# Performance work log

Hardware: AMD Instinct MI355X
Metric: run time of the kernel (lower is better)

## Reference

```python
import jax, jax.numpy as jnp
import numpy as np

D_MODEL = 1024
HEADS = 16


def setup_inputs() -> dict:
    key = jax.random.key(0)
    ks = jax.random.split(key, 5)
    S = 4096
    x = jax.random.normal(ks[0], (S, D_MODEL), dtype=jnp.float32)
    scale = 1.0 / np.sqrt(D_MODEL)
    Wq = jax.random.normal(ks[1], (D_MODEL, D_MODEL), dtype=jnp.float32) * scale
    Wk = jax.random.normal(ks[2], (D_MODEL, D_MODEL), dtype=jnp.float32) * scale
    Wv = jax.random.normal(ks[3], (D_MODEL, D_MODEL), dtype=jnp.float32) * scale
    Wo = jax.random.normal(ks[4], (D_MODEL, D_MODEL), dtype=jnp.float32) * scale
    return {"x": x, "Wq": Wq, "Wk": Wk, "Wv": Wv, "Wo": Wo}


def reference(x, Wq, Wk, Wv, Wo):
    # x: [S, D]; weights follow torch Linear convention y = x @ W.T
    S, D = x.shape
    H = HEADS
    d_k = D // H
    q = (x @ Wq.T).reshape(S, H, d_k)  # [S,H,dk]
    k = (x @ Wk.T).reshape(S, H, d_k)
    v = (x @ Wv.T).reshape(S, H, d_k)
    # logits: [H, S, S] = q k^T / sqrt(d_k)
    logits = jnp.einsum('shd,thd->hst', q, k) / jnp.sqrt(jnp.asarray(d_k, x.dtype))
    probs = jax.nn.softmax(logits, axis=-1)
    out = jnp.einsum('hst,thd->shd', probs, v).reshape(S, D)
    return out @ Wo.T
```

## Files before the change

kernel.cpp:

```cpp
#include <hip/hip_runtime.h>
#include <hip/hip_bf16.h>


typedef __bf16 bf16_t;
typedef __bf16 bf16x8 __attribute__((ext_vector_type(8)));
typedef __bf16 bf16x4 __attribute__((ext_vector_type(4)));
typedef float f32x4 __attribute__((ext_vector_type(4)));

#define D_MODEL 1024
#define SEQ 4096
#define HEADS 16
#define DK 64
#define QSCALE 0.1803368801111204f

__global__ void cast_kernel(const float* __restrict__ in, bf16_t* __restrict__ out, int n) {
    int i = (blockIdx.x * blockDim.x + threadIdx.x) * 4;
    if (i < n) {
        float4 v = *(const float4*)(in + i);
        bf16x4 o;
        o[0] = (bf16_t)v.x; o[1] = (bf16_t)v.y; o[2] = (bf16_t)v.z; o[3] = (bf16_t)v.w;
        *(bf16x4*)(out + i) = o;
    }
}

__global__ void cast4_kernel(const float* __restrict__ a, const float* __restrict__ b,
                             const float* __restrict__ c, const float* __restrict__ d,
                             bf16_t* __restrict__ out) {
    int gi = blockIdx.x * blockDim.x + threadIdx.x;
    int which = gi >> 18;
    int i = (gi & 0x3FFFF) * 4;
    const float* src = which == 0 ? a : which == 1 ? b : which == 2 ? c : d;
    float4 v = *(const float4*)(src + i);
    bf16x4 o;
    o[0] = (bf16_t)v.x; o[1] = (bf16_t)v.y; o[2] = (bf16_t)v.z; o[3] = (bf16_t)v.w;
    *(bf16x4*)(out + (size_t)which * D_MODEL * D_MODEL + i) = o;
}

__device__ __forceinline__ void g2l16(const bf16_t* g, bf16_t* l) {
    __builtin_amdgcn_global_load_lds(
        (const __attribute__((address_space(1))) void*)g,
        (__attribute__((address_space(3))) void*)l, 16, 0, 0);
}

template <int ROUTE>
__global__ __launch_bounds__(256, 4) void gemm_lds(const bf16_t* __restrict__ A,
                                                   const bf16_t* __restrict__ B,
                                                   void* __restrict__ out0,
                                                   void* __restrict__ out1,
                                                   void* __restrict__ out2,
                                                   int M, int N, int K) {
    __shared__ __align__(16) bf16_t As[128 * 64];
    __shared__ __align__(16) bf16_t Bs[64 * 64];

    const int tid = threadIdx.x;
    const int lane = tid & 63;
    const int wave = tid >> 6;
    const int l15 = lane & 15;
    const int lg  = lane >> 4;
    const int m0 = blockIdx.y * 128;
    const int n0 = blockIdx.x * 64;
    const int wm = (wave >> 1) * 64;
    const int wn = (wave & 1) * 32;

    const bf16_t* aSrc[4]; bf16_t* aDst[4];
#pragma unroll
    for (int it = 0; it < 4; it++) {
        int c = it * 256 + tid;
        int row = c >> 3, cc = (c & 7) ^ (row & 7);
        aSrc[it] = A + (size_t)(m0 + row) * K + cc * 8;
        aDst[it] = As + c * 8;
    }
    const bf16_t* bSrc[2]; bf16_t* bDst[2];
#pragma unroll
    for (int it = 0; it < 2; it++) {
        int c = it * 256 + tid;
        int row = c >> 3, cc = (c & 7) ^ (row & 7);
        bSrc[it] = B + (size_t)(n0 + row) * K + cc * 8;
        bDst[it] = Bs + c * 8;
    }

    int aoff[2][4], boff[2][2];
#pragma unroll
    for (int kk = 0; kk < 2; kk++) {
#pragma unroll
        for (int i = 0; i < 4; i++) {
            int row = wm + i * 16 + l15;
            aoff[kk][i] = row * 64 + (((kk << 2) | lg) ^ (row & 7)) * 8;
        }
#pragma unroll
        for (int j = 0; j < 2; j++) {
            int row = wn + j * 16 + l15;
            boff[kk][j] = row * 64 + (((kk << 2) | lg) ^ (row & 7)) * 8;
        }
    }

    f32x4 acc[4][2];
#pragma unroll
    for (int i = 0; i < 4; i++)
#pragma unroll
        for (int j = 0; j < 2; j++) acc[i][j] = f32x4{0.f, 0.f, 0.f, 0.f};

    for (int k0 = 0; k0 < K; k0 += 64) {
#pragma unroll
        for (int it = 0; it < 4; it++) g2l16(aSrc[it] + k0, aDst[it]);
#pragma unroll
        for (int it = 0; it < 2; it++) g2l16(bSrc[it] + k0, bDst[it]);
        __syncthreads();

#pragma unroll
        for (int kk = 0; kk < 2; kk++) {
            bf16x8 af[4], bfm[2];
#pragma unroll
            for (int i = 0; i < 4; i++) af[i] = *(const bf16x8*)(As + aoff[kk][i]);
#pragma unroll
            for (int j = 0; j < 2; j++) bfm[j] = *(const bf16x8*)(Bs + boff[kk][j]);
#pragma unroll
            for (int i = 0; i < 4; i++)
#pragma unroll
                for (int j = 0; j < 2; j++)
                    acc[i][j] = __builtin_amdgcn_mfma_f32_16x16x32_bf16(af[i], bfm[j], acc[i][j], 0, 0, 0);
        }
        __syncthreads();
    }

    const int ng = n0 + wn;
    if (ROUTE == 0) {
        float* C = (float*)out0;
#pragma unroll
        for (int i = 0; i < 4; i++)
#pragma unroll
            for (int r = 0; r < 4; r++) {
                int m = m0 + wm + i * 16 + lg * 4 + r;
                float* crow = C + (size_t)m * N + ng;
#pragma unroll
                for (int j = 0; j < 2; j++) crow[j * 16 + l15] = acc[i][j][r];
            }
    } else {
        if (ng < 2048) {
            const bool isQ = (ng < 1024);
            const float sc = isQ ? QSCALE : 1.0f;
            bf16_t* dst = isQ ? (bf16_t*)out0 : (bf16_t*)out1;
            int nn = ng & 1023;
#pragma unroll
            for (int i = 0; i < 4; i++)
#pragma unroll
                for (int r = 0; r < 4; r++) {
                    int m = m0 + wm + i * 16 + lg * 4 + r;
                    bf16_t* crow = dst + (size_t)m * D_MODEL + nn;
#pragma unroll
                    for (int j = 0; j < 2; j++) crow[j * 16 + l15] = (bf16_t)(acc[i][j][r] * sc);
                }
        } else {
            bf16_t* Vt = (bf16_t*)out2;
#pragma unroll
            for (int i = 0; i < 4; i++)
#pragma unroll
                for (int j = 0; j < 2; j++) {
                    int vcol = ng - 2048 + j * 16 + l15;
                    int m = m0 + wm + i * 16 + lg * 4;
                    bf16x4 v4;
#pragma unroll
                    for (int r = 0; r < 4; r++) v4[r] = (bf16_t)acc[i][j][r];
                    *(bf16x4*)(Vt + (size_t)vcol * SEQ + m) = v4;
                }
        }
    }
}

__global__ __launch_bounds__(256) void attn_kernel(const bf16_t* __restrict__ Q,
                                                   const bf16_t* __restrict__ Km,
                                                   const bf16_t* __restrict__ Vt,
                                                   bf16_t* __restrict__ O) {
    const int tid = threadIdx.x;
    const int lane = tid & 63;
    const int wave = tid >> 6;
    const int l15 = lane & 15;
    const int lg  = lane >> 4;
    const int bid = blockIdx.x;
    const int h    = (bid & 7) * 2 + ((bid >> 3) & 1);
    const int qblk = bid >> 4;
    const int q0 = qblk * 128;
    const int hoff = h * DK;

    __shared__ union {
        struct { __align__(16) bf16_t K[64 * 64]; __align__(16) bf16_t V[64 * 64]; } kv;
        __align__(16) bf16_t Ot[128][72];
    } sm;

    bf16x8 qf[2][2];
#pragma unroll
    for (int t = 0; t < 2; t++)
#pragma unroll
        for (int c = 0; c < 2; c++)
            qf[t][c] = *(const bf16x8*)(Q + (size_t)(q0 + wave * 32 + t * 16 + l15) * D_MODEL
                                        + hoff + c * 32 + lg * 8);

    f32x4 oacc[2][4], lfrag[2];
#pragma unroll
    for (int t = 0; t < 2; t++) {
        lfrag[t] = f32x4{0.f, 0.f, 0.f, 0.f};
#pragma unroll
        for (int dt = 0; dt < 4; dt++) oacc[t][dt] = f32x4{0.f, 0.f, 0.f, 0.f};
    }

    bf16x8 ones8;
#pragma unroll
    for (int j = 0; j < 8; j++) ones8[j] = (bf16_t)1.0f;

    const bf16_t* kSrc[2]; const bf16_t* vSrc[2];
#pragma unroll
    for (int it = 0; it < 2; it++) {
        int c = it * 256 + tid;
        int row = c >> 3, dc = (c & 7) ^ (row & 7);
        kSrc[it] = Km + (size_t)row * D_MODEL + hoff + dc * 8;
        vSrc[it] = Vt + (size_t)(hoff + row) * SEQ + dc * 8;
    }

    int kOff[4][2], vOff[2][2][4];
#pragma unroll
    for (int kt = 0; kt < 4; kt++)
#pragma unroll
        for (int c = 0; c < 2; c++) {
            int row = kt * 16 + l15;
            kOff[kt][c] = row * 64 + (((c * 4 + lg) ^ (row & 7)) * 8);
        }
#pragma unroll
    for (int kp = 0; kp < 2; kp++)
#pragma unroll
        for (int hf = 0; hf < 2; hf++)
#pragma unroll
            for (int dt = 0; dt < 4; dt++) {
                int row = dt * 16 + l15;
                vOff[kp][hf][dt] = row * 64 + (((kp * 4 + hf * 2 + (lg >> 1)) ^ (row & 7)) * 8)
                                   + (lg & 1) * 4;
            }

    for (int s = 0; s < SEQ / 64; s++) {
#pragma unroll
        for (int it = 0; it < 2; it++) {
            g2l16(kSrc[it] + (size_t)s * 64 * D_MODEL, sm.kv.K + (it * 256 + tid) * 8);
            g2l16(vSrc[it] + s * 64,                   sm.kv.V + (it * 256 + tid) * 8);
        }
        __syncthreads();

#pragma unroll
        for (int kp = 0; kp < 2; kp++) {
            f32x4 st[2][2];
#pragma unroll
            for (int sub = 0; sub < 2; sub++) {
                const int kt = kp * 2 + sub;
                const bf16x8 kf0 = *(const bf16x8*)(sm.kv.K + kOff[kt][0]);
                const bf16x8 kf1 = *(const bf16x8*)(sm.kv.K + kOff[kt][1]);
#pragma unroll
                for (int t = 0; t < 2; t++) {
                    f32x4 a = f32x4{0.f, 0.f, 0.f, 0.f};
                    a = __builtin_amdgcn_mfma_f32_16x16x32_bf16(kf0, qf[t][0], a, 0, 0, 0);
                    a = __builtin_amdgcn_mfma_f32_16x16x32_bf16(kf1, qf[t][1], a, 0, 0, 0);
                    st[t][sub] = a;
                }
            }

            bf16x8 pbig[2];
#pragma unroll
            for (int t = 0; t < 2; t++) {
#pragma unroll
                for (int r = 0; r < 4; r++) {
                    pbig[t][r]     = (bf16_t)__builtin_amdgcn_exp2f(st[t][0][r]);
                    pbig[t][r + 4] = (bf16_t)__builtin_amdgcn_exp2f(st[t][1][r]);
                }
            }

            lfrag[0] = __builtin_amdgcn_mfma_f32_16x16x32_bf16(ones8, pbig[0], lfrag[0], 0, 0, 0);
            lfrag[1] = __builtin_amdgcn_mfma_f32_16x16x32_bf16(ones8, pbig[1], lfrag[1], 0, 0, 0);

#pragma unroll
            for (int dt = 0; dt < 4; dt++) {
                const bf16x4 v0 = *(const bf16x4*)(sm.kv.V + vOff[kp][0][dt]);
                const bf16x4 v1 = *(const bf16x4*)(sm.kv.V + vOff[kp][1][dt]);
                bf16x8 vf;
#pragma unroll
                for (int j = 0; j < 4; j++) { vf[j] = v0[j]; vf[j + 4] = v1[j]; }
                oacc[0][dt] = __builtin_amdgcn_mfma_f32_16x16x32_bf16(vf, pbig[0], oacc[0][dt], 0, 0, 0);
                oacc[1][dt] = __builtin_amdgcn_mfma_f32_16x16x32_bf16(vf, pbig[1], oacc[1][dt], 0, 0, 0);
            }
        }
        __syncthreads();
    }

#pragma unroll
    for (int t = 0; t < 2; t++) {
        float inv = 1.f / lfrag[t][0];
        const int qrow = wave * 32 + t * 16 + l15;
#pragma unroll
        for (int dt = 0; dt < 4; dt++)
#pragma unroll
            for (int r = 0; r < 4; r++)
                sm.Ot[qrow][dt * 16 + lg * 4 + r] = (bf16_t)(oacc[t][dt][r] * inv);
    }
    __syncthreads();

    {
        const int row = tid >> 1;
        const int half = tid & 1;
        bf16_t* orow = O + (size_t)(q0 + row) * D_MODEL + hoff + half * 32;
#pragma unroll
        for (int m = 0; m < 4; m++)
            *(bf16x8*)(orow + m * 8) = *(const bf16x8*)(&sm.Ot[row][half * 32 + m * 8]);
    }
}

extern "C" void kernel_launch(void* const* d_in, const int* in_sizes, int n_in,
                              void* d_out, int out_size, void* d_ws, size_t ws_size,
                              hipStream_t stream) {
    const float* x  = (const float*)d_in[0];
    const float* Wq = (const float*)d_in[1];
    const float* Wk = (const float*)d_in[2];
    const float* Wv = (const float*)d_in[3];
    const float* Wo = (const float*)d_in[4];
    float* out = (float*)d_out;

    char* ws = (char*)d_ws;
    bf16_t* xb  = (bf16_t*)(ws);
    bf16_t* wqb = (bf16_t*)(ws + (8u  << 20));
    bf16_t* wob = (bf16_t*)(ws + (14u << 20));
    bf16_t* Qb  = (bf16_t*)(ws + (16u << 20));
    bf16_t* Kb  = (bf16_t*)(ws + (24u << 20));
    bf16_t* Vtb = (bf16_t*)(ws + (32u << 20));
    bf16_t* Ab  = (bf16_t*)(ws + (40u << 20));

    const int nX = SEQ * D_MODEL;
    cast_kernel<<<nX / 4 / 256, 256, 0, stream>>>(x, xb, nX);
    cast4_kernel<<<4 * 1024, 256, 0, stream>>>(Wq, Wk, Wv, Wo, wqb);

    gemm_lds<1><<<dim3(3 * D_MODEL / 64, SEQ / 128), 256, 0, stream>>>(
        xb, wqb, Qb, Kb, Vtb, SEQ, 3 * D_MODEL, D_MODEL);

    attn_kernel<<<512, 256, 0, stream>>>(Qb, Kb, Vtb, Ab);

    gemm_lds<0><<<dim3(D_MODEL / 64, SEQ / 128), 256, 0, stream>>>(
        Ab, wob, out, nullptr, nullptr, SEQ, D_MODEL, D_MODEL);
}
```

Baseline: 226.5 us.

## Split attention over key halves and combine partial outputs in separate kernel

Each attention block now handles only half of the key sequence, doubling the grid to 1024 blocks. Unnormalized partial outputs (bf16) and row sums (fp32) go to workspace, and a new combine kernel adds them, normalizes, and writes the attention output. This is meant to raise occupancy and shorten each block's serial key loop. In exchange it adds an extra launch, extra global traffic for the partials, and bf16 rounding of unnormalized partials.

After: 235.0 us. 1.04x slower.

```diff
diff --git a/kernel.cpp b/kernel.cpp
--- a/kernel.cpp
+++ b/kernel.cpp
@@ -170,7 +170,8 @@
 __global__ __launch_bounds__(256) void attn_kernel(const bf16_t* __restrict__ Q,
                                                    const bf16_t* __restrict__ Km,
                                                    const bf16_t* __restrict__ Vt,
-                                                   bf16_t* __restrict__ O) {
+                                                   bf16_t* __restrict__ Opart,
+                                                   float* __restrict__ Lpart) {
     const int tid = threadIdx.x;
     const int lane = tid & 63;
     const int wave = tid >> 6;
@@ -178,14 +179,13 @@
     const int lg  = lane >> 4;
     const int bid = blockIdx.x;
     const int h    = (bid & 7) * 2 + ((bid >> 3) & 1);
-    const int qblk = bid >> 4;
+    const int ks   = (bid >> 4) & 1;
+    const int qblk = bid >> 5;
+    const int cid  = (bid & 15) | (qblk << 4);
     const int q0 = qblk * 128;
     const int hoff = h * DK;
 
-    __shared__ union {
-        struct { __align__(16) bf16_t K[64 * 64]; __align__(16) bf16_t V[64 * 64]; } kv;
-        __align__(16) bf16_t Ot[128][72];
-    } sm;
+    __shared__ struct { __align__(16) bf16_t K[64 * 64]; __align__(16) bf16_t V[64 * 64]; } sm;
 
     bf16x8 qf[2][2];
 #pragma unroll
@@ -235,11 +235,11 @@
                                    + (lg & 1) * 4;
             }
 
-    for (int s = 0; s < SEQ / 64; s++) {
+    for (int s = ks * 32; s < ks * 32 + 32; s++) {
 #pragma unroll
         for (int it = 0; it < 2; it++) {
-            g2l16(kSrc[it] + (size_t)s * 64 * D_MODEL, sm.kv.K + (it * 256 + tid) * 8);
-            g2l16(vSrc[it] + s * 64,                   sm.kv.V + (it * 256 + tid) * 8);
+            g2l16(kSrc[it] + (size_t)s * 64 * D_MODEL, sm.K + (it * 256 + tid) * 8);
+            g2l16(vSrc[it] + s * 64,                   sm.V + (it * 256 + tid) * 8);
         }
         __syncthreads();
 
@@ -249,8 +249,8 @@
 #pragma unroll
             for (int sub = 0; sub < 2; sub++) {
                 const int kt = kp * 2 + sub;
-                const bf16x8 kf0 = *(const bf16x8*)(sm.kv.K + kOff[kt][0]);
-                const bf16x8 kf1 = *(const bf16x8*)(sm.kv.K + kOff[kt][1]);
+                const bf16x8 kf0 = *(const bf16x8*)(sm.K + kOff[kt][0]);
+                const bf16x8 kf1 = *(const bf16x8*)(sm.K + kOff[kt][1]);
 #pragma unroll
                 for (int t = 0; t < 2; t++) {
                     f32x4 a = f32x4{0.f, 0.f, 0.f, 0.f};
@@ -275,8 +275,8 @@
 
 #pragma unroll
             for (int dt = 0; dt < 4; dt++) {
-                const bf16x4 v0 = *(const bf16x4*)(sm.kv.V + vOff[kp][0][dt]);
-                const bf16x4 v1 = *(const bf16x4*)(sm.kv.V + vOff[kp][1][dt]);
+                const bf16x4 v0 = *(const bf16x4*)(sm.V + vOff[kp][0][dt]);
+                const bf16x4 v1 = *(const bf16x4*)(sm.V + vOff[kp][1][dt]);
                 bf16x8 vf;
 #pragma unroll
                 for (int j = 0; j < 4; j++) { vf[j] = v0[j]; vf[j + 4] = v1[j]; }
@@ -288,25 +288,64 @@
     }
 
 #pragma unroll
+    for (int dt = 0; dt < 4; dt++) {
+        bf16x8 pk;
+#pragma unroll
+        for (int r = 0; r < 4; r++) {
+            pk[r]     = (bf16_t)oacc[0][dt][r];
+            pk[r + 4] = (bf16_t)oacc[1][dt][r];
+        }
+        *(bf16x8*)(Opart + ((size_t)((ks * 512 + cid) * 4 + dt) * 256 + tid) * 8) = pk;
+    }
+    if (lg == 0) {
+#pragma unroll
+        for (int t = 0; t < 2; t++)
+            Lpart[(ks * 512 + cid) * 128 + wave * 32 + t * 16 + l15] = lfrag[t][0];
+    }
+}
+
+__global__ __launch_bounds__(256) void attn_combine(const bf16_t* __restrict__ Opart,
+                                                    const float* __restrict__ Lpart,
+                                                    bf16_t* __restrict__ O) {
+    __shared__ __align__(16) bf16_t Ot[128][72];
+    const int tid = threadIdx.x;
+    const int lane = tid & 63;
+    const int wave = tid >> 6;
+    const int l15 = lane & 15;
+    const int lg  = lane >> 4;
+    const int cid = blockIdx.x;
+    const int h    = (cid & 7) * 2 + ((cid >> 3) & 1);
+    const int qblk = cid >> 4;
+    const int q0 = qblk * 128;
+    const int hoff = h * DK;
+
+    float inv[2];
+#pragma unroll
     for (int t = 0; t < 2; t++) {
-        float inv = 1.f / lfrag[t][0];
-        const int qrow = wave * 32 + t * 16 + l15;
-#pragma unroll
-        for (int dt = 0; dt < 4; dt++)
-#pragma unroll
-            for (int r = 0; r < 4; r++)
-                sm.Ot[qrow][dt * 16 + lg * 4 + r] = (bf16_t)(oacc[t][dt][r] * inv);
+        int q = wave * 32 + t * 16 + l15;
+        inv[t] = 1.f / (Lpart[cid * 128 + q] + Lpart[(512 + cid) * 128 + q]);
+    }
+
+#pragma unroll
+    for (int dt = 0; dt < 4; dt++) {
+        const bf16x8 a = *(const bf16x8*)(Opart + ((size_t)(cid * 4 + dt) * 256 + tid) * 8);
+        const bf16x8 b = *(const bf16x8*)(Opart + ((size_t)((512 + cid) * 4 + dt) * 256 + tid) * 8);
+#pragma unroll
+        for (int r = 0; r < 4; r++) {
+            float v0 = (float)a[r] + (float)b[r];
+            float v1 = (float)a[r + 4] + (float)b[r + 4];
+            Ot[wave * 32 + l15][dt * 16 + lg * 4 + r]      = (bf16_t)(v0 * inv[0]);
+            Ot[wave * 32 + 16 + l15][dt * 16 + lg * 4 + r] = (bf16_t)(v1 * inv[1]);
+        }
     }
     __syncthreads();
 
-    {
-        const int row = tid >> 1;
-        const int half = tid & 1;
-        bf16_t* orow = O + (size_t)(q0 + row) * D_MODEL + hoff + half * 32;
-#pragma unroll
-        for (int m = 0; m < 4; m++)
-            *(bf16x8*)(orow + m * 8) = *(const bf16x8*)(&sm.Ot[row][half * 32 + m * 8]);
-    }
+    const int row = tid >> 1;
+    const int half = tid & 1;
+    bf16_t* orow = O + (size_t)(q0 + row) * D_MODEL + hoff + half * 32;
+#pragma unroll
+    for (int m = 0; m < 4; m++)
+        *(bf16x8*)(orow + m * 8) = *(const bf16x8*)(&Ot[row][half * 32 + m * 8]);
 }
 
 extern "C" void kernel_launch(void* const* d_in, const int* in_sizes, int n_in,
@@ -320,13 +359,15 @@
     float* out = (float*)d_out;
 
     char* ws = (char*)d_ws;
-    bf16_t* xb  = (bf16_t*)(ws);
-    bf16_t* wqb = (bf16_t*)(ws + (8u  << 20));
-    bf16_t* wob = (bf16_t*)(ws + (14u << 20));
-    bf16_t* Qb  = (bf16_t*)(ws + (16u << 20));
-    bf16_t* Kb  = (bf16_t*)(ws + (24u << 20));
-    bf16_t* Vtb = (bf16_t*)(ws + (32u << 20));
-    bf16_t* Ab  = (bf16_t*)(ws + (40u << 20));
+    bf16_t* xb    = (bf16_t*)(ws);
+    bf16_t* Ab    = (bf16_t*)(ws);
+    bf16_t* wqb   = (bf16_t*)(ws + (8u  << 20));
+    bf16_t* wob   = (bf16_t*)(ws + (14u << 20));
+    bf16_t* Qb    = (bf16_t*)(ws + (16u << 20));
+    bf16_t* Kb    = (bf16_t*)(ws + (24u << 20));
+    bf16_t* Vtb   = (bf16_t*)(ws + (32u << 20));
+    bf16_t* Opart = (bf16_t*)(ws + (40u << 20));
+    float*  Lpart = (float*) (ws + (56u << 20));
 
     const int nX = SEQ * D_MODEL;
     cast_kernel<<<nX / 4 / 256, 256, 0, stream>>>(x, xb, nX);
@@ -335,7 +376,8 @@
     gemm_lds<1><<<dim3(3 * D_MODEL / 64, SEQ / 128), 256, 0, stream>>>(
         xb, wqb, Qb, Kb, Vtb, SEQ, 3 * D_MODEL, D_MODEL);
 
-    attn_kernel<<<512, 256, 0, stream>>>(Qb, Kb, Vtb, Ab);
+    attn_kernel<<<1024, 256, 0, stream>>>(Qb, Kb, Vtb, Opart, Lpart);
+    attn_combine<<<512, 256, 0, stream>>>(Opart, Lpart, Ab);
 
     gemm_lds<0><<<dim3(D_MODEL / 64, SEQ / 128), 256, 0, stream>>>(
         Ab, wob, out, nullptr, nullptr, SEQ, D_MODEL, D_MODEL);
```

## Merge cast kernels and give QKV GEMM its own 128x128 tile kernel

Applied to the files above, without the earlier changes.

The two fp32-to-bf16 cast launches become a single kernel covering x and all four weights, which saves one launch. The QKV projection moves to a dedicated kernel with a 128x128 tile, so each wave holds a 64x64 accumulator (16 MFMA tiles) and A and B LDS loads get more reuse. The output GEMM keeps the old 128x64 tiling. The larger tile raises register and LDS use and lowers occupancy, and the grid falls to 768 blocks.

New measurement: 232.1 us. 1.02x slower.

```diff
diff --git a/kernel.cpp b/kernel.cpp
--- a/kernel.cpp
+++ b/kernel.cpp
@@ -13,27 +13,25 @@
 #define DK 64
 #define QSCALE 0.1803368801111204f
 
-__global__ void cast_kernel(const float* __restrict__ in, bf16_t* __restrict__ out, int n) {
-    int i = (blockIdx.x * blockDim.x + threadIdx.x) * 4;
-    if (i < n) {
-        float4 v = *(const float4*)(in + i);
-        bf16x4 o;
-        o[0] = (bf16_t)v.x; o[1] = (bf16_t)v.y; o[2] = (bf16_t)v.z; o[3] = (bf16_t)v.w;
-        *(bf16x4*)(out + i) = o;
-    }
-}
-
-__global__ void cast4_kernel(const float* __restrict__ a, const float* __restrict__ b,
-                             const float* __restrict__ c, const float* __restrict__ d,
-                             bf16_t* __restrict__ out) {
+__global__ void cast_all(const float* __restrict__ x,
+                         const float* __restrict__ a, const float* __restrict__ b,
+                         const float* __restrict__ c, const float* __restrict__ d,
+                         bf16_t* __restrict__ xb, bf16_t* __restrict__ wb) {
     int gi = blockIdx.x * blockDim.x + threadIdx.x;
-    int which = gi >> 18;
-    int i = (gi & 0x3FFFF) * 4;
-    const float* src = which == 0 ? a : which == 1 ? b : which == 2 ? c : d;
+    const float* src; bf16_t* dst; int i;
+    if (gi < (1 << 20)) {
+        i = gi * 4; src = x; dst = xb;
+    } else {
+        int g2 = gi - (1 << 20);
+        int which = g2 >> 18;
+        i = (g2 & 0x3FFFF) * 4;
+        src = which == 0 ? a : which == 1 ? b : which == 2 ? c : d;
+        dst = wb + (size_t)which * D_MODEL * D_MODEL;
+    }
     float4 v = *(const float4*)(src + i);
     bf16x4 o;
     o[0] = (bf16_t)v.x; o[1] = (bf16_t)v.y; o[2] = (bf16_t)v.z; o[3] = (bf16_t)v.w;
-    *(bf16x4*)(out + (size_t)which * D_MODEL * D_MODEL + i) = o;
+    *(bf16x4*)(dst + i) = o;
 }
 
 __device__ __forceinline__ void g2l16(const bf16_t* g, bf16_t* l) {
@@ -42,12 +40,112 @@
         (__attribute__((address_space(3))) void*)l, 16, 0, 0);
 }
 
-template <int ROUTE>
-__global__ __launch_bounds__(256, 4) void gemm_lds(const bf16_t* __restrict__ A,
+__global__ __launch_bounds__(256) void gemm_qkv(const bf16_t* __restrict__ A,
+                                                const bf16_t* __restrict__ B,
+                                                bf16_t* __restrict__ Qo,
+                                                bf16_t* __restrict__ Ko,
+                                                bf16_t* __restrict__ Vt) {
+    __shared__ __align__(16) bf16_t As[128 * 64];
+    __shared__ __align__(16) bf16_t Bs[128 * 64];
+
+    const int tid = threadIdx.x;
+    const int lane = tid & 63;
+    const int wave = tid >> 6;
+    const int l15 = lane & 15;
+    const int lg  = lane >> 4;
+    const int m0 = blockIdx.y * 128;
+    const int n0 = blockIdx.x * 128;
+    const int wm = (wave >> 1) * 64;
+    const int wn = (wave & 1) * 64;
+    const int K = D_MODEL;
+
+    const bf16_t* aSrc[4]; bf16_t* aDst[4];
+    const bf16_t* bSrc[4]; bf16_t* bDst[4];
+#pragma unroll
+    for (int it = 0; it < 4; it++) {
+        int c = it * 256 + tid;
+        int row = c >> 3, cc = (c & 7) ^ (row & 7);
+        aSrc[it] = A + (size_t)(m0 + row) * K + cc * 8;
+        aDst[it] = As + c * 8;
+        bSrc[it] = B + (size_t)(n0 + row) * K + cc * 8;
+        bDst[it] = Bs + c * 8;
+    }
+
+    int aoff[2][4], boff[2][4];
+#pragma unroll
+    for (int kk = 0; kk < 2; kk++)
+#pragma unroll
+        for (int i = 0; i < 4; i++) {
+            int ra = wm + i * 16 + l15;
+            aoff[kk][i] = ra * 64 + (((kk * 4 + lg) ^ (ra & 7)) * 8);
+            int rb = wn + i * 16 + l15;
+            boff[kk][i] = rb * 64 + (((kk * 4 + lg) ^ (rb & 7)) * 8);
+        }
+
+    f32x4 acc[4][4];
+#pragma unroll
+    for (int i = 0; i < 4; i++)
+#pragma unroll
+        for (int j = 0; j < 4; j++) acc[i][j] = f32x4{0.f, 0.f, 0.f, 0.f};
+
+    for (int k0 = 0; k0 < K; k0 += 64) {
+#pragma unroll
+        for (int it = 0; it < 4; it++) {
+            g2l16(aSrc[it] + k0, aDst[it]);
+            g2l16(bSrc[it] + k0, bDst[it]);
+        }
+        __syncthreads();
+
+#pragma unroll
+        for (int kk = 0; kk < 2; kk++) {
+            bf16x8 af[4], bfm[4];
+#pragma unroll
+            for (int i = 0; i < 4; i++) af[i] = *(const bf16x8*)(As + aoff[kk][i]);
+#pragma unroll
+            for (int j = 0; j < 4; j++) bfm[j] = *(const bf16x8*)(Bs + boff[kk][j]);
+#pragma unroll
+            for (int i = 0; i < 4; i++)
+#pragma unroll
+                for (int j = 0; j < 4; j++)
+                    acc[i][j] = __builtin_amdgcn_mfma_f32_16x16x32_bf16(af[i], bfm[j], acc[i][j], 0, 0, 0);
+        }
+        __syncthreads();
+    }
+
+    const int bx = blockIdx.x;
+    if (bx < 16) {
+        const bool isQ = (bx < 8);
+        const float sc = isQ ? QSCALE : 1.0f;
+        bf16_t* dst = isQ ? Qo : Ko;
+        const int nn = (n0 & 1023) + wn;
+#pragma unroll
+        for (int i = 0; i < 4; i++)
+#pragma unroll
+            for (int r = 0; r < 4; r++) {
+                int m = m0 + wm + i * 16 + lg * 4 + r;
+                bf16_t* crow = dst + (size_t)m * D_MODEL + nn;
+#pragma unroll
+                for (int j = 0; j < 4; j++) crow[j * 16 + l15] = (bf16_t)(acc[i][j][r] * sc);
+            }
+    } else {
+        const int nb = n0 - 2048 + wn;
+#pragma unroll
+        for (int i = 0; i < 4; i++)
+#pragma unroll
+            for (int j = 0; j < 4; j++) {
+                int vcol = nb + j * 16 + l15;
+                int m = m0 + wm + i * 16 + lg * 4;
+                bf16x4 v4;
+#pragma unroll
+                for (int r = 0; r < 4; r++) v4[r] = (bf16_t)acc[i][j][r];
+                *(bf16x4*)(Vt + (size_t)vcol * SEQ + m) = v4;
+            }
+    }
+}
+
+__global__ __launch_bounds__(256, 4) void gemm_out(const bf16_t* __restrict__ A,
                                                    const bf16_t* __restrict__ B,
-                                                   void* __restrict__ out0,
-                                                   void* __restrict__ out1,
-                                                   void* __restrict__ out2,
+                                                   float* __restrict__ C,
                                                    int M, int N, int K) {
     __shared__ __align__(16) bf16_t As[128 * 64];
     __shared__ __align__(16) bf16_t Bs[64 * 64];
@@ -123,48 +221,15 @@
         __syncthreads();
     }
 
-    const int ng = n0 + wn;
-    if (ROUTE == 0) {
-        float* C = (float*)out0;
-#pragma unroll
-        for (int i = 0; i < 4; i++)
-#pragma unroll
-            for (int r = 0; r < 4; r++) {
-                int m = m0 + wm + i * 16 + lg * 4 + r;
-                float* crow = C + (size_t)m * N + ng;
-#pragma unroll
-                for (int j = 0; j < 2; j++) crow[j * 16 + l15] = acc[i][j][r];
-            }
-    } else {
-        if (ng < 2048) {
-            const bool isQ = (ng < 1024);
-            const float sc = isQ ? QSCALE : 1.0f;
-            bf16_t* dst = isQ ? (bf16_t*)out0 : (bf16_t*)out1;
-            int nn = ng & 1023;
-#pragma unroll
-            for (int i = 0; i < 4; i++)
-#pragma unroll
-                for (int r = 0; r < 4; r++) {
-                    int m = m0 + wm + i * 16 + lg * 4 + r;
-                    bf16_t* crow = dst + (size_t)m * D_MODEL + nn;
-#pragma unroll
-                    for (int j = 0; j < 2; j++) crow[j * 16 + l15] = (bf16_t)(acc[i][j][r] * sc);
-                }
-        } else {
-            bf16_t* Vt = (bf16_t*)out2;
-#pragma unroll
-            for (int i = 0; i < 4; i++)
-#pragma unroll
-                for (int j = 0; j < 2; j++) {
-                    int vcol = ng - 2048 + j * 16 + l15;
-                    int m = m0 + wm + i * 16 + lg * 4;
-                    bf16x4 v4;
-#pragma unroll
-                    for (int r = 0; r < 4; r++) v4[r] = (bf16_t)acc[i][j][r];
-                    *(bf16x4*)(Vt + (size_t)vcol * SEQ + m) = v4;
-                }
-        }
-    }
+#pragma unroll
+    for (int i = 0; i < 4; i++)
+#pragma unroll
+        for (int r = 0; r < 4; r++) {
+            int m = m0 + wm + i * 16 + lg * 4 + r;
+            float* crow = C + (size_t)m * N + n0 + wn;
+#pragma unroll
+            for (int j = 0; j < 2; j++) crow[j * 16 + l15] = acc[i][j][r];
+        }
 }
 
 __global__ __launch_bounds__(256) void attn_kernel(const bf16_t* __restrict__ Q,
@@ -262,13 +327,12 @@
 
             bf16x8 pbig[2];
 #pragma unroll
-            for (int t = 0; t < 2; t++) {
+            for (int t = 0; t < 2; t++)
 #pragma unroll
                 for (int r = 0; r < 4; r++) {
                     pbig[t][r]     = (bf16_t)__builtin_amdgcn_exp2f(st[t][0][r]);
                     pbig[t][r + 4] = (bf16_t)__builtin_amdgcn_exp2f(st[t][1][r]);
                 }
-            }
 
             lfrag[0] = __builtin_amdgcn_mfma_f32_16x16x32_bf16(ones8, pbig[0], lfrag[0], 0, 0, 0);
             lfrag[1] = __builtin_amdgcn_mfma_f32_16x16x32_bf16(ones8, pbig[1], lfrag[1], 0, 0, 0);
@@ -328,15 +392,13 @@
     bf16_t* Vtb = (bf16_t*)(ws + (32u << 20));
     bf16_t* Ab  = (bf16_t*)(ws + (40u << 20));
 
-    const int nX = SEQ * D_MODEL;
-    cast_kernel<<<nX / 4 / 256, 256, 0, stream>>>(x, xb, nX);
-    cast4_kernel<<<4 * 1024, 256, 0, stream>>>(Wq, Wk, Wv, Wo, wqb);
-
-    gemm_lds<1><<<dim3(3 * D_MODEL / 64, SEQ / 128), 256, 0, stream>>>(
-        xb, wqb, Qb, Kb, Vtb, SEQ, 3 * D_MODEL, D_MODEL);
+    cast_all<<<8192, 256, 0, stream>>>(x, Wq, Wk, Wv, Wo, xb, wqb);
+
+    gemm_qkv<<<dim3(3 * D_MODEL / 128, SEQ / 128), 256, 0, stream>>>(
+        xb, wqb, Qb, Kb, Vtb);
 
     attn_kernel<<<512, 256, 0, stream>>>(Qb, Kb, Vtb, Ab);
 
-    gemm_lds<0><<<dim3(D_MODEL / 64, SEQ / 128), 256, 0, stream>>>(
-        Ab, wob, out, nullptr, nullptr, SEQ, D_MODEL, D_MODEL);
-}
+    gemm_out<<<dim3(D_MODEL / 64, SEQ / 128), 256, 0, stream>>>(
+        Ab, wob, out, SEQ, D_MODEL, D_MODEL);
+}
```
